# Kernel tuning notes

Hardware: AMD Instinct MI355X
Metric: run time of the kernel (lower is better)

The kernel has to match this reference:

```python
import jax, jax.numpy as jnp
import numpy as np

NUM_ITERS = 5
GKS, GSIG = 5, 0.1          # spatial gaussian conv kernel
BKS, BSSIG, BCSIG = 5, 5.0, 0.1  # bilateral window / spatial sigma / color sigma


def gaussian_kernel(k, sigma):
    ax = jnp.arange(k, dtype=jnp.float32) - (k - 1) / 2
    xx, yy = jnp.meshgrid(ax, ax, indexing='ij')
    kern = jnp.exp(-(xx ** 2 + yy ** 2) / (2 * sigma ** 2))
    return kern / kern.sum()


def unfold(x, k):
    # x: [B,C,H,W] -> [B,C,K2,H,W], patch index ordered row-major like F.unfold
    B, C, H, W = x.shape
    p = k // 2
    xp = jnp.pad(x, ((0, 0), (0, 0), (p, p), (p, p)))
    return jnp.stack([xp[:, :, i:i + H, j:j + W]
                      for i in range(k) for j in range(k)], axis=2)


def setup_inputs() -> dict:
    key = jax.random.key(0)
    k1, k2, k3 = jax.random.split(key, 3)
    B, C, H, W = 2, 21, 256, 256
    logits = jax.random.normal(k1, (B, C, H, W), jnp.float32)
    img = jax.random.uniform(k2, (B, 3, H, W), jnp.float32)
    gt_edges = jax.random.uniform(k3, (B, H, W), jnp.float32)
    compat_mat = -jnp.eye(C, dtype=jnp.float32)  # nn.Parameter init: -kappa*I
    return {"logits": logits, "img": img, "gt_edges": gt_edges,
            "compat_mat": compat_mat}


def reference(logits, img, gt_edges, compat_mat):
    B, C, H, W = logits.shape
    q = jax.nn.softmax(logits, axis=1)

    gk = gaussian_kernel(GKS, GSIG).reshape(1, 1, GKS, GKS)
    pad_g = GKS // 2
    K2 = BKS * BKS
    spatial_w = gaussian_kernel(BKS, BSSIG).reshape(1, 1, K2, 1, 1)

    # bilateral color weights depend only on img -> hoisted out of the loop
    img_unf = unfold(img, BKS)                       # [B,3,K2,H,W]
    diff = img_unf - img[:, :, None]                 # center = img itself
    color_w = jnp.exp(-(diff ** 2).sum(1, keepdims=True) / (2 * BCSIG ** 2))
    w = spatial_w * color_w                          # [B,1,K2,H,W]

    for _ in range(NUM_ITERS):
        # spatial gaussian filtering of q (depthwise via batched single-channel conv)
        sp = jax.lax.conv_general_dilated(
            q.reshape(B * C, 1, H, W), gk, (1, 1),
            [(pad_g, pad_g), (pad_g, pad_g)],
            dimension_numbers=('NCHW', 'OIHW', 'NCHW')).reshape(B, C, H, W)
        # bilateral message passing over the local window
        q_unf = unfold(q, BKS)                       # [B,C,K2,H,W]
        bilateral_rgb = (q_unf * w).sum(2)           # [B,C,H,W]
        # compatibility transform + mean-field update
        pairwise = jnp.einsum('ij,bjhw->bihw', compat_mat, sp + bilateral_rgb)
        q = jax.nn.softmax(logits - pairwise, axis=1)
    # note: original also computes bilateral_edge = q * conv(gt_edges) but it is
    # dead code (never used in pairwise or output), so it is omitted here.
    return q
```

## Files before the change

kernel.cpp:

```cpp
#include <hip/hip_runtime.h>
#include <hip/hip_fp16.h>

constexpr int Bn = 2, C = 21, H = 256, W = 256, HW = H * W;
constexpr int K2 = 25;
constexpr int CQ = 6;
constexpr int TW = 32, TH = 16, NT = 1024;
constexpr int HALO = 10;
constexpr int EH = TH + 2 * HALO;
constexpr int EW = TW + 2 * HALO;
constexpr int NEC = EH * EW;

__device__ constexpr float SKN[K2] = {
    0.03688346f, 0.03916421f, 0.03995538f, 0.03916421f, 0.03688346f,
    0.03916421f, 0.04158598f, 0.04242608f, 0.04158598f, 0.03916421f,
    0.03995538f, 0.04242608f, 0.04328314f, 0.04242608f, 0.03995538f,
    0.03916421f, 0.04158598f, 0.04242608f, 0.04158598f, 0.03916421f,
    0.03688346f, 0.03916421f, 0.03995538f, 0.03916421f, 0.03688346f};

union H2U { __half2 h; unsigned int u; };

template <int MARGIN, bool FINAL>
__device__ __forceinline__ void mf_iter(
        int tid, int b, int y0, int x0, int fast,
        const float* __restrict__ lgb, const float* __restrict__ scm,
        __half2 (*bufQ)[EH][EW][2], const float4* simg,
        float* __restrict__ outp) {
    constexpr int HT_ = EH - 2 * MARGIN, WT_ = EW - 2 * MARGIN;
    constexpr int NCEL = HT_ * WT_;
    constexpr int NS = (NCEL + NT - 1) / NT;
    unsigned int nq[NS][12];
    bool valid[NS];
#pragma unroll
    for (int s = 0; s < NS; ++s) {
        valid[s] = false;
        const int cell = tid + s * NT;
        if (cell < NCEL) {
            const int ry = cell / WT_, rx = cell % WT_;
            const int ey = MARGIN + ry, ex = MARGIN + rx;
            const int gy = y0 + ey - HALO, gx = x0 + ex - HALO;
            if ((unsigned)gy < H && (unsigned)gx < W) {
                valid[s] = true;
                const float* lgp = lgb + gy * W + gx;
                float lg[C];
#pragma unroll
                for (int c = 0; c < C; ++c) lg[c] = lgp[(size_t)c * HW];
                const float4 ctr = simg[ey * EW + ex];
                unsigned int wk[K2];
#pragma unroll
                for (int k = 0; k < K2; ++k) {
                    const int dy = k / 5 - 2, dx = k % 5 - 2;
                    const float4 nb = simg[(ey + dy) * EW + (ex + dx)];
                    const float d0 = nb.x - ctr.x, d1 = nb.y - ctr.y,
                                d2 = nb.z - ctr.z;
                    float wv = SKN[k] *
                        __expf(-50.f * (d0 * d0 + d1 * d1 + d2 * d2));
                    if (k == 12) wv += 1.0f;
                    H2U cv; cv.h = __float2half2_rn(wv);
                    wk[k] = cv.u;
                }
                const __half2 zero2 = __float2half2_rn(0.f);
                __half2 aA[CQ][2], aB[CQ][2];
#pragma unroll
                for (int g = 0; g < CQ; ++g) {
                    aA[g][0] = zero2; aA[g][1] = zero2;
                    aB[g][0] = zero2; aB[g][1] = zero2;
                }
#pragma unroll
                for (int k = 0; k < K2; ++k) {
                    const int ly = ey + k / 5 - 2, lx = ex + k % 5 - 2;
                    H2U wv; wv.u = wk[k];
#pragma unroll
                    for (int g = 0; g < CQ; ++g) {
                        const uint2 raw =
                            *reinterpret_cast<const uint2*>(&bufQ[g][ly][lx][0]);
                        H2U q01, q23; q01.u = raw.x; q23.u = raw.y;
                        if (k < 13) {
                            aA[g][0] = __hfma2(wv.h, q01.h, aA[g][0]);
                            aA[g][1] = __hfma2(wv.h, q23.h, aA[g][1]);
                        } else {
                            aB[g][0] = __hfma2(wv.h, q01.h, aB[g][0]);
                            aB[g][1] = __hfma2(wv.h, q23.h, aB[g][1]);
                        }
                    }
                }
                float m[24];
#pragma unroll
                for (int g = 0; g < CQ; ++g) {
                    const float2 lA = __half22float2(aA[g][0]);
                    const float2 lB = __half22float2(aB[g][0]);
                    const float2 hA = __half22float2(aA[g][1]);
                    const float2 hB = __half22float2(aB[g][1]);
                    m[4 * g + 0] = lA.x + lB.x;
                    m[4 * g + 1] = lA.y + lB.y;
                    m[4 * g + 2] = hA.x + hB.x;
                    m[4 * g + 3] = hA.y + hB.y;
                }
                float z[C], mx = -1e30f;
                if (fast) {
#pragma unroll
                    for (int c = 0; c < C; ++c) {
                        z[c] = lg[c] + m[c]; mx = fmaxf(mx, z[c]);
                    }
                } else {
#pragma unroll
                    for (int c = 0; c < C; ++c) {
                        float pw = 0.f;
#pragma unroll
                        for (int j = 0; j < C; ++j) pw += scm[c * C + j] * m[j];
                        z[c] = lg[c] - pw; mx = fmaxf(mx, z[c]);
                    }
                }
                float ssum = 0.f;
#pragma unroll
                for (int c = 0; c < C; ++c) {
                    z[c] = __expf(z[c] - mx); ssum += z[c];
                }
                const float inv = 1.f / ssum;
                if (FINAL) {
                    float* qo = outp + (size_t)b * C * HW + gy * W + gx;
#pragma unroll
                    for (int c = 0; c < C; ++c) qo[(size_t)c * HW] = z[c] * inv;
                } else {
                    float vals[24];
#pragma unroll
                    for (int c = 0; c < 24; ++c)
                        vals[c] = (c < C) ? z[c] * inv : 0.f;
#pragma unroll
                    for (int g = 0; g < CQ; ++g) {
                        H2U p0; p0.h = __floats2half2_rn(vals[4 * g + 0], vals[4 * g + 1]);
                        H2U p1; p1.h = __floats2half2_rn(vals[4 * g + 2], vals[4 * g + 3]);
                        nq[s][2 * g + 0] = p0.u;
                        nq[s][2 * g + 1] = p1.u;
                    }
                }
            }
        }
    }
    if (!FINAL) {
        __syncthreads();
#pragma unroll
        for (int s = 0; s < NS; ++s) {
            if (valid[s]) {
                const int cell = tid + s * NT;
                const int ry = cell / WT_, rx = cell % WT_;
                const int ey = MARGIN + ry, ex = MARGIN + rx;
#pragma unroll
                for (int g = 0; g < CQ; ++g)
                    *reinterpret_cast<uint2*>(&bufQ[g][ey][ex][0]) =
                        make_uint2(nq[s][2 * g], nq[s][2 * g + 1]);
            }
        }
        __syncthreads();
    }
}

__global__ __launch_bounds__(NT, 4) void crf_mega(
        const float* __restrict__ logits, const float* __restrict__ img,
        const float* __restrict__ compat, float* __restrict__ out) {
    __shared__ __align__(16) __half2 bufQ[CQ][EH][EW][2];
    __shared__ __align__(16) float4 simg[NEC];
    __shared__ float scm[C * C];

    const int b = blockIdx.z;
    const int x0 = blockIdx.x * TW, y0 = blockIdx.y * TH;
    const int tid = threadIdx.x;

    int ok = 1;
    for (int i = tid; i < C * C; i += NT) {
        const float v = compat[i];
        scm[i] = v;
        ok &= (v == ((i / C == i % C) ? -1.0f : 0.0f));
    }

    const float* im  = img + (size_t)b * 3 * HW;
    const float* lgb = logits + (size_t)b * C * HW;

    for (int cell = tid; cell < NEC; cell += NT) {
        const int ey = cell / EW, ex = cell % EW;
        const int gy = y0 + ey - HALO, gx = x0 + ex - HALO;
        float4 iv = make_float4(0.f, 0.f, 0.f, 0.f);
        float vals[24];
        if ((unsigned)gy < H && (unsigned)gx < W) {
            const int np = gy * W + gx;
            iv.x = im[np]; iv.y = im[HW + np]; iv.z = im[2 * HW + np];
            const float* lg = lgb + np;
            float zz[C], mx = -1e30f;
#pragma unroll
            for (int c = 0; c < C; ++c) {
                zz[c] = lg[(size_t)c * HW]; mx = fmaxf(mx, zz[c]);
            }
            float ssum = 0.f;
#pragma unroll
            for (int c = 0; c < C; ++c) { zz[c] = __expf(zz[c] - mx); ssum += zz[c]; }
            const float inv = 1.f / ssum;
#pragma unroll
            for (int c = 0; c < 24; ++c) vals[c] = (c < C) ? zz[c] * inv : 0.f;
        } else {
#pragma unroll
            for (int c = 0; c < 24; ++c) vals[c] = 0.f;
        }
        simg[cell] = iv;
#pragma unroll
        for (int g = 0; g < CQ; ++g) {
            bufQ[g][ey][ex][0] = __floats2half2_rn(vals[4 * g + 0], vals[4 * g + 1]);
            bufQ[g][ey][ex][1] = __floats2half2_rn(vals[4 * g + 2], vals[4 * g + 3]);
        }
    }
    const int fast = __syncthreads_and(ok);

    mf_iter< 2, false>(tid, b, y0, x0, fast, lgb, scm, bufQ, simg, out);
    mf_iter< 4, false>(tid, b, y0, x0, fast, lgb, scm, bufQ, simg, out);
    mf_iter< 6, false>(tid, b, y0, x0, fast, lgb, scm, bufQ, simg, out);
    mf_iter< 8, false>(tid, b, y0, x0, fast, lgb, scm, bufQ, simg, out);
    mf_iter<10, true >(tid, b, y0, x0, fast, lgb, scm, bufQ, simg, out);
}

extern "C" void kernel_launch(void* const* d_in, const int* in_sizes, int n_in,
                              void* d_out, int out_size, void* d_ws, size_t ws_size,
                              hipStream_t stream) {
    const float* logits = (const float*)d_in[0];
    const float* img    = (const float*)d_in[1];
    const float* compat = (const float*)d_in[3];
    float* out = (float*)d_out;

    dim3 g(W / TW, H / TH, Bn);
    crf_mega<<<g, NT, 0, stream>>>(logits, img, compat, out);
}
```

Before: 58.92 us.

## Split fused five-iteration CRF kernel into two phases with smaller halos

The single mega-kernel, which ran all five mean-field iterations on a tile with a 10-pixel halo, is replaced by two launches. The first runs three iterations with a 6-pixel halo and writes q to workspace; the second reloads q and runs two iterations with a 4-pixel halo. Tiles shrink to 32x8 with 512 threads, which cuts redundant halo recomputation and shared memory per block and gives more blocks. The cost is an extra launch and a global round trip of the full q tensor between phases.

```diff
diff --git a/kernel.cpp b/kernel.cpp
--- a/kernel.cpp
+++ b/kernel.cpp
@@ -2,15 +2,10 @@
 #include <hip/hip_fp16.h>
 
 constexpr int Bn = 2, C = 21, H = 256, W = 256, HW = H * W;
-constexpr int K2 = 25;
 constexpr int CQ = 6;
-constexpr int TW = 32, TH = 16, NT = 1024;
-constexpr int HALO = 10;
-constexpr int EH = TH + 2 * HALO;
-constexpr int EW = TW + 2 * HALO;
-constexpr int NEC = EH * EW;
-
-__device__ constexpr float SKN[K2] = {
+constexpr int TW = 32, THt = 8, NT = 512;
+
+__device__ constexpr float SKN[25] = {
     0.03688346f, 0.03916421f, 0.03995538f, 0.03916421f, 0.03688346f,
     0.03916421f, 0.04158598f, 0.04242608f, 0.04158598f, 0.03916421f,
     0.03995538f, 0.04242608f, 0.04328314f, 0.04242608f, 0.03995538f,
@@ -19,13 +14,14 @@
 
 union H2U { __half2 h; unsigned int u; };
 
-template <int MARGIN, bool FINAL>
+template <int EHp, int EWp, int MARGIN, bool FINAL>
 __device__ __forceinline__ void mf_iter(
         int tid, int b, int y0, int x0, int fast,
         const float* __restrict__ lgb, const float* __restrict__ scm,
-        __half2 (*bufQ)[EH][EW][2], const float4* simg,
+        __half2 (*bufQ)[EHp][EWp][2], const float4* __restrict__ simg,
         float* __restrict__ outp) {
-    constexpr int HT_ = EH - 2 * MARGIN, WT_ = EW - 2 * MARGIN;
+    constexpr int HALOP = (EHp - THt) / 2;
+    constexpr int HT_ = EHp - 2 * MARGIN, WT_ = EWp - 2 * MARGIN;
     constexpr int NCEL = HT_ * WT_;
     constexpr int NS = (NCEL + NT - 1) / NT;
     unsigned int nq[NS][12];
@@ -37,19 +33,19 @@
         if (cell < NCEL) {
             const int ry = cell / WT_, rx = cell % WT_;
             const int ey = MARGIN + ry, ex = MARGIN + rx;
-            const int gy = y0 + ey - HALO, gx = x0 + ex - HALO;
+            const int gy = y0 + ey - HALOP, gx = x0 + ex - HALOP;
             if ((unsigned)gy < H && (unsigned)gx < W) {
                 valid[s] = true;
                 const float* lgp = lgb + gy * W + gx;
                 float lg[C];
 #pragma unroll
                 for (int c = 0; c < C; ++c) lg[c] = lgp[(size_t)c * HW];
-                const float4 ctr = simg[ey * EW + ex];
-                unsigned int wk[K2];
-#pragma unroll
-                for (int k = 0; k < K2; ++k) {
+                const float4 ctr = simg[ey * EWp + ex];
+                unsigned int wk[25];
+#pragma unroll
+                for (int k = 0; k < 25; ++k) {
                     const int dy = k / 5 - 2, dx = k % 5 - 2;
-                    const float4 nb = simg[(ey + dy) * EW + (ex + dx)];
+                    const float4 nb = simg[(ey + dy) * EWp + (ex + dx)];
                     const float d0 = nb.x - ctr.x, d1 = nb.y - ctr.y,
                                 d2 = nb.z - ctr.z;
                     float wv = SKN[k] *
@@ -66,7 +62,7 @@
                     aB[g][0] = zero2; aB[g][1] = zero2;
                 }
 #pragma unroll
-                for (int k = 0; k < K2; ++k) {
+                for (int k = 0; k < 25; ++k) {
                     const int ly = ey + k / 5 - 2, lx = ex + k % 5 - 2;
                     H2U wv; wv.u = wk[k];
 #pragma unroll
@@ -154,15 +150,19 @@
     }
 }
 
-__global__ __launch_bounds__(NT, 4) void crf_mega(
-        const float* __restrict__ logits, const float* __restrict__ img,
-        const float* __restrict__ compat, float* __restrict__ out) {
-    __shared__ __align__(16) __half2 bufQ[CQ][EH][EW][2];
-    __shared__ __align__(16) float4 simg[NEC];
+template <int HALOP, bool INIT, int NIT>
+__global__ __launch_bounds__(NT, 4) void crf_phase(
+        const float* __restrict__ qin, const float* __restrict__ logits,
+        const float* __restrict__ img, const float* __restrict__ compat,
+        float* __restrict__ qout) {
+    constexpr int EHp = THt + 2 * HALOP, EWp = TW + 2 * HALOP;
+    constexpr int NECp = EHp * EWp;
+    __shared__ __align__(16) __half2 bufQ[CQ][EHp][EWp][2];
+    __shared__ __align__(16) float4 simg[NECp];
     __shared__ float scm[C * C];
 
     const int b = blockIdx.z;
-    const int x0 = blockIdx.x * TW, y0 = blockIdx.y * TH;
+    const int x0 = blockIdx.x * TW, y0 = blockIdx.y * THt;
     const int tid = threadIdx.x;
 
     int ok = 1;
@@ -175,26 +175,33 @@
     const float* im  = img + (size_t)b * 3 * HW;
     const float* lgb = logits + (size_t)b * C * HW;
 
-    for (int cell = tid; cell < NEC; cell += NT) {
-        const int ey = cell / EW, ex = cell % EW;
-        const int gy = y0 + ey - HALO, gx = x0 + ex - HALO;
+    for (int cell = tid; cell < NECp; cell += NT) {
+        const int ey = cell / EWp, ex = cell % EWp;
+        const int gy = y0 + ey - HALOP, gx = x0 + ex - HALOP;
         float4 iv = make_float4(0.f, 0.f, 0.f, 0.f);
         float vals[24];
         if ((unsigned)gy < H && (unsigned)gx < W) {
             const int np = gy * W + gx;
             iv.x = im[np]; iv.y = im[HW + np]; iv.z = im[2 * HW + np];
-            const float* lg = lgb + np;
-            float zz[C], mx = -1e30f;
-#pragma unroll
-            for (int c = 0; c < C; ++c) {
-                zz[c] = lg[(size_t)c * HW]; mx = fmaxf(mx, zz[c]);
+            if (INIT) {
+                const float* lg = lgb + np;
+                float zz[C], mx = -1e30f;
+#pragma unroll
+                for (int c = 0; c < C; ++c) {
+                    zz[c] = lg[(size_t)c * HW]; mx = fmaxf(mx, zz[c]);
+                }
+                float ssum = 0.f;
+#pragma unroll
+                for (int c = 0; c < C; ++c) { zz[c] = __expf(zz[c] - mx); ssum += zz[c]; }
+                const float inv = 1.f / ssum;
+#pragma unroll
+                for (int c = 0; c < 24; ++c) vals[c] = (c < C) ? zz[c] * inv : 0.f;
+            } else {
+                const float* qp = qin + (size_t)b * C * HW + np;
+#pragma unroll
+                for (int c = 0; c < 24; ++c)
+                    vals[c] = (c < C) ? qp[(size_t)c * HW] : 0.f;
             }
-            float ssum = 0.f;
-#pragma unroll
-            for (int c = 0; c < C; ++c) { zz[c] = __expf(zz[c] - mx); ssum += zz[c]; }
-            const float inv = 1.f / ssum;
-#pragma unroll
-            for (int c = 0; c < 24; ++c) vals[c] = (c < C) ? zz[c] * inv : 0.f;
         } else {
 #pragma unroll
             for (int c = 0; c < 24; ++c) vals[c] = 0.f;
@@ -208,11 +215,11 @@
     }
     const int fast = __syncthreads_and(ok);
 
-    mf_iter< 2, false>(tid, b, y0, x0, fast, lgb, scm, bufQ, simg, out);
-    mf_iter< 4, false>(tid, b, y0, x0, fast, lgb, scm, bufQ, simg, out);
-    mf_iter< 6, false>(tid, b, y0, x0, fast, lgb, scm, bufQ, simg, out);
-    mf_iter< 8, false>(tid, b, y0, x0, fast, lgb, scm, bufQ, simg, out);
-    mf_iter<10, true >(tid, b, y0, x0, fast, lgb, scm, bufQ, simg, out);
+    mf_iter<EHp, EWp, 2, (NIT == 1)>(tid, b, y0, x0, fast, lgb, scm, bufQ, simg, qout);
+    if constexpr (NIT >= 2)
+        mf_iter<EHp, EWp, 4, (NIT == 2)>(tid, b, y0, x0, fast, lgb, scm, bufQ, simg, qout);
+    if constexpr (NIT >= 3)
+        mf_iter<EHp, EWp, 6, (NIT == 3)>(tid, b, y0, x0, fast, lgb, scm, bufQ, simg, qout);
 }
 
 extern "C" void kernel_launch(void* const* d_in, const int* in_sizes, int n_in,
@@ -222,7 +229,9 @@
     const float* img    = (const float*)d_in[1];
     const float* compat = (const float*)d_in[3];
     float* out = (float*)d_out;
-
-    dim3 g(W / TW, H / TH, Bn);
-    crf_mega<<<g, NT, 0, stream>>>(logits, img, compat, out);
+    float* q3  = (float*)d_ws;
+
+    dim3 g(W / TW, H / THt, Bn);
+    crf_phase<6, true, 3><<<g, NT, 0, stream>>>(nullptr, logits, img, compat, q3);
+    crf_phase<4, false, 2><<<g, NT, 0, stream>>>(q3, logits, img, compat, out);
 }
```

New measurement: 61.78 us. 4.9% more time.
